# Optimization experiments

Measured on AMD Instinct MI355X. Metric: run time of the kernel, lower is better.

Reference implementation:

```python
import jax, jax.numpy as jnp
import numpy as np

N_NODES = 100000
N_EDGES = 1600000
IN_FEATS = 128
OUT_FEATS = 64


def setup_inputs() -> dict:
    key = jax.random.key(0)
    k1, k2, k3, k4 = jax.random.split(key, 4)
    feat = jax.random.normal(k1, (N_NODES, IN_FEATS), dtype=jnp.float32)
    W = jax.random.normal(k2, (IN_FEATS, OUT_FEATS), dtype=jnp.float32) * (1.0 / np.sqrt(IN_FEATS))
    src = jax.random.randint(k3, (N_EDGES,), 0, N_NODES, dtype=jnp.int64)
    dst = jax.random.randint(k4, (N_EDGES,), 0, N_NODES, dtype=jnp.int64)
    return {"feat": feat, "W": W, "src": src, "dst": dst}


def reference(feat, W, src, dst):
    # Linear projection (bias=False): homogeneous graph -> shared fc
    ft = feat @ W  # [N, out]

    # per-edge dot-product score: e_ij = <ft[src], ft[dst]>
    a = jnp.sum(ft[src] * ft[dst], axis=-1)  # [E]

    # edge softmax segmented by destination node (numerically stable)
    neg_inf = jnp.finfo(a.dtype).min
    m = jax.ops.segment_max(a, dst, num_segments=N_NODES)  # [N]
    m = jnp.where(m == neg_inf, 0.0, m)  # guard zero-in-degree nodes
    e = jnp.exp(a - m[dst])  # [E]
    s = jax.ops.segment_sum(e, dst, num_segments=N_NODES)  # [N]
    s = jnp.where(s == 0.0, 1.0, s)
    sa = e / s[dst]  # [E]

    # weighted scatter-sum aggregation: out[i] = sum_{j in N(i)} sa_ij * ft[j]
    rst = jax.ops.segment_sum(ft[src] * sa[:, None], dst, num_segments=N_NODES)
    return rst
```

## Files before the change

kernel.cpp:

```cpp
#include <hip/hip_runtime.h>
#include <hip/hip_fp16.h>
#include <math.h>

#define N_NODES 100000
#define N_EDGES 1600000
#define IN_F    128
#define OUT_F   64
#define K_BKT     196
#define BKT_SHIFT 9
#define BKT_NODES 512
#define BKT_CAP   10240
#define CHUNK     4096
#define PBLKS     ((N_EDGES + CHUNK - 1) / CHUNK)
#define LTILES    (N_NODES / 16)
#define LBLKS     ((LTILES + 3) / 4)

typedef _Float16 half8 __attribute__((ext_vector_type(8)));
typedef _Float16 h2 __attribute__((ext_vector_type(2)));
typedef _Float16 h4 __attribute__((ext_vector_type(4)));
typedef __fp16   q2v __attribute__((ext_vector_type(2)));
typedef float    f32x4 __attribute__((ext_vector_type(4)));

__device__ __forceinline__ float fdot2f(h2 a, h2 b, float c) {
#if __has_builtin(__builtin_amdgcn_fdot2)
    return __builtin_amdgcn_fdot2(__builtin_bit_cast(q2v, a), __builtin_bit_cast(q2v, b), c, false);
#else
    return (float)a[0] * (float)b[0] + (float)a[1] * (float)b[1] + c;
#endif
}

#if __has_builtin(__builtin_amdgcn_update_dpp)
#define DPP_ADD(x, ctrl)                                                                  \
    (x) += __builtin_bit_cast(float, __builtin_amdgcn_update_dpp(                         \
               0, __builtin_bit_cast(int, (x)), (ctrl), 0xF, 0xF, true))
#define REDUCE16(x) do { DPP_ADD(x, 0xB1); DPP_ADD(x, 0x4E); \
                         DPP_ADD(x, 0x141); DPP_ADD(x, 0x140); } while (0)
#else
#define REDUCE16(x) do { x += __shfl_xor(x, 1); x += __shfl_xor(x, 2); \
                         x += __shfl_xor(x, 4); x += __shfl_xor(x, 8); } while (0)
#endif


__global__ __launch_bounds__(256) void partition_linear_kernel(const int* __restrict__ src,
                                                               const int* __restrict__ dst,
                                                               unsigned* __restrict__ staging,
                                                               int* __restrict__ pcnt,
                                                               int* __restrict__ pbase,
                                                               const float* __restrict__ feat,
                                                               const float* __restrict__ W,
                                                               __half* __restrict__ fth) {
    __shared__ int hist[256], lbase[256], sc[256];
    __shared__ unsigned sval[CHUNK];
    int t = threadIdx.x;
    if (blockIdx.x < PBLKS) {
        hist[t] = 0;
        __syncthreads();
        int beg = blockIdx.x * CHUNK;
        int end = min(beg + CHUNK, N_EDGES);
        for (int i = beg + t; i < end; i += 256)
            atomicAdd(&hist[dst[i] >> BKT_SHIFT], 1);
        __syncthreads();
        int v = hist[t];
        sc[t] = v;
        __syncthreads();
        for (int off = 1; off < 256; off <<= 1) {
            int add = (t >= off) ? sc[t - off] : 0;
            __syncthreads();
            sc[t] += add;
            __syncthreads();
        }
        int lb = sc[t] - v;
        lbase[t] = lb;
        pcnt[blockIdx.x * 256 + t]  = v;
        pbase[blockIdx.x * 256 + t] = lb;
        hist[t] = 0;
        __syncthreads();
        for (int i = beg + t; i < end; i += 256) {
            int s = src[i], d = dst[i];
            int b = d >> BKT_SHIFT;
            int r = atomicAdd(&hist[b], 1);
            sval[lbase[b] + r] = (unsigned)s | ((unsigned)(d & (BKT_NODES - 1)) << 17);
        }
        __syncthreads();
        int n = end - beg;
        for (int p = t; p < n; p += 256)
            staging[(size_t)blockIdx.x * CHUNK + p] = sval[p];
        return;
    }
    int gwave = (blockIdx.x - PBLKS) * 4 + (t >> 6);
    if (gwave >= LTILES) return;
    int lane = t & 63;
    int m = lane & 15, kg = lane >> 4;
    int r0 = gwave * 16;

    half8 fb[4][4];
#pragma unroll
    for (int kb = 0; kb < 4; ++kb)
#pragma unroll
        for (int nb = 0; nb < 4; ++nb) {
            const float* wp = W + (size_t)(kb * 32 + kg * 8) * OUT_F + nb * 16 + m;
#pragma unroll
            for (int j = 0; j < 8; ++j)
                fb[kb][nb][j] = (_Float16)wp[j * OUT_F];
        }

    f32x4 acc[4];
#pragma unroll
    for (int nb = 0; nb < 4; ++nb) acc[nb] = (f32x4){0.f, 0.f, 0.f, 0.f};

#pragma unroll
    for (int kb = 0; kb < 4; ++kb) {
        const float4* ap = (const float4*)(feat + (size_t)(r0 + m) * IN_F + kb * 32 + kg * 8);
        float4 a0 = ap[0], a1 = ap[1];
        half8 fa = {(_Float16)a0.x, (_Float16)a0.y, (_Float16)a0.z, (_Float16)a0.w,
                    (_Float16)a1.x, (_Float16)a1.y, (_Float16)a1.z, (_Float16)a1.w};
#pragma unroll
        for (int nb = 0; nb < 4; ++nb)
            acc[nb] = __builtin_amdgcn_mfma_f32_16x16x32_f16(fa, fb[kb][nb], acc[nb], 0, 0, 0);
    }
#pragma unroll
    for (int nb = 0; nb < 4; ++nb)
#pragma unroll
        for (int i = 0; i < 4; ++i)
            fth[(size_t)(r0 + kg * 4 + i) * OUT_F + nb * 16 + m] = __float2half_rn(acc[nb][i]);
}

__global__ __launch_bounds__(1024) void place_kernel(const unsigned* __restrict__ staging,
                                                     const int* __restrict__ pcnt,
                                                     const int* __restrict__ pbase,
                                                     int* __restrict__ row_beg,
                                                     int* __restrict__ row_end,
                                                     int* __restrict__ edge_src) {
    __shared__ unsigned sbuf[BKT_CAP];
    __shared__ int exo[PBLKS];
    __shared__ int pbs[PBLKS];
    __shared__ int scnt[PBLKS];
    __shared__ int s512[512];
    __shared__ int cnt[BKT_NODES], lcur[BKT_NODES];
    __shared__ int ntot;
    int t = threadIdx.x;
    int b = blockIdx.x;

    int d = 0;
    if (t < PBLKS) { d = pcnt[t * 256 + b]; pbs[t] = pbase[t * 256 + b]; scnt[t] = d; }
    if (t < 512) { s512[t] = (t < PBLKS) ? d : 0; cnt[t] = 0; }
    __syncthreads();
    for (int off = 1; off < 512; off <<= 1) {
        int add = (t >= off && t < 512) ? s512[t - off] : 0;
        __syncthreads();
        if (t < 512) s512[t] += add;
        __syncthreads();
    }
    if (t < PBLKS) exo[t] = s512[t] - d;
    if (t == PBLKS - 1) ntot = s512[t];
    __syncthreads();
    int n = ntot;

    {
        int wid = t >> 6, ln = t & 63;
        for (int s = wid; s < PBLKS; s += 16) {
            int c = scnt[s], eo = exo[s];
            size_t gb = (size_t)s * CHUNK + pbs[s];
            for (int j = ln; j < c; j += 64)
                sbuf[eo + j] = staging[gb + j];
        }
    }
    __syncthreads();
    for (int i = t; i < n; i += 1024)
        atomicAdd(&cnt[sbuf[i] >> 17], 1);
    __syncthreads();
    int v = (t < 512) ? cnt[t] : 0;
    if (t < 512) s512[t] = v;
    __syncthreads();
    for (int off = 1; off < 512; off <<= 1) {
        int add = (t >= off && t < 512) ? s512[t - off] : 0;
        __syncthreads();
        if (t < 512) s512[t] += add;
        __syncthreads();
    }
    if (t < 512) {
        int b0 = b * BKT_CAP + s512[t] - v;
        lcur[t] = b0;
        int node = b * BKT_NODES + t;
        if (node < N_NODES) { row_beg[node] = b0; row_end[node] = b0 + v; }
    }
    __syncthreads();
    for (int i = t; i < n; i += 1024) {
        unsigned u = sbuf[i];
        int pos = atomicAdd(&lcur[u >> 17], 1);
        edge_src[pos] = (int)(u & 0x1FFFFu);
    }
}

__global__ __launch_bounds__(256) void fused_node_kernel(const __half* __restrict__ fth,
                                                         const int* __restrict__ row_beg,
                                                         const int* __restrict__ row_end,
                                                         const int* __restrict__ edge_src,
                                                         float* __restrict__ out) {
    const float LOG2E = 1.44269504088896340736f;
    int wave = (blockIdx.x * 256 + threadIdx.x) >> 6;
    int lane = threadIdx.x & 63;
    if (wave >= N_NODES) return;
    int q = lane >> 4, ql = lane & 15;

    int beg = row_beg[wave];
    int end = row_end[wave];

    const _Float16* fh = (const _Float16*)fth;
    h4 rdv = *(const h4*)(fh + (size_t)wave * OUT_F + 4 * ql);
    h2 dlo = __builtin_shufflevector(rdv, rdv, 0, 1);
    h2 dhi = __builtin_shufflevector(rdv, rdv, 2, 3);

    float m = -1e30f, l = 0.f;
    float a0 = 0.f, a1 = 0.f, a2 = 0.f, a3 = 0.f;

    for (int i = beg; i < end; i += 16) {
        int e0 = i + q, e1 = e0 + 4, e2 = e0 + 8, e3 = e0 + 12;
        bool u0 = e0 < end, u1 = e1 < end, u2 = e2 < end, u3 = e3 < end;
        int s0 = edge_src[u0 ? e0 : beg];
        int s1 = edge_src[u1 ? e1 : beg];
        int s2 = edge_src[u2 ? e2 : beg];
        int s3 = edge_src[u3 ? e3 : beg];
        h4 rA = *(const h4*)(fh + (size_t)s0 * OUT_F + 4 * ql);
        h4 rB = *(const h4*)(fh + (size_t)s1 * OUT_F + 4 * ql);
        h4 rC = *(const h4*)(fh + (size_t)s2 * OUT_F + 4 * ql);
        h4 rD = *(const h4*)(fh + (size_t)s3 * OUT_F + 4 * ql);

        float p0 = fdot2f(__builtin_shufflevector(rA, rA, 0, 1), dlo,
                   fdot2f(__builtin_shufflevector(rA, rA, 2, 3), dhi, 0.f));
        float p1 = fdot2f(__builtin_shufflevector(rB, rB, 0, 1), dlo,
                   fdot2f(__builtin_shufflevector(rB, rB, 2, 3), dhi, 0.f));
        float p2 = fdot2f(__builtin_shufflevector(rC, rC, 0, 1), dlo,
                   fdot2f(__builtin_shufflevector(rC, rC, 2, 3), dhi, 0.f));
        float p3 = fdot2f(__builtin_shufflevector(rD, rD, 0, 1), dlo,
                   fdot2f(__builtin_shufflevector(rD, rD, 2, 3), dhi, 0.f));
        REDUCE16(p0);
        REDUCE16(p1);
        REDUCE16(p2);
        REDUCE16(p3);
        p0 = u0 ? p0 * LOG2E : -1e30f;
        p1 = u1 ? p1 * LOG2E : -1e30f;
        p2 = u2 ? p2 * LOG2E : -1e30f;
        p3 = u3 ? p3 * LOG2E : -1e30f;

        float nm = fmaxf(fmaxf(fmaxf(p0, p1), fmaxf(p2, p3)), m);
        float alpha = exp2f(m - nm);
        float w0 = exp2f(p0 - nm), w1 = exp2f(p1 - nm);
        float w2 = exp2f(p2 - nm), w3 = exp2f(p3 - nm);
        l = l * alpha + ((w0 + w1) + (w2 + w3));
#if __has_builtin(__builtin_amdgcn_cvt_pkrtz)
        h2 wlo = __builtin_bit_cast(h2, __builtin_amdgcn_cvt_pkrtz(w0, w1));
        h2 whi = __builtin_bit_cast(h2, __builtin_amdgcn_cvt_pkrtz(w2, w3));
#else
        h2 wlo = {(_Float16)w0, (_Float16)w1};
        h2 whi = {(_Float16)w2, (_Float16)w3};
#endif
        h2 cab0 = {rA[0], rB[0]}, ccd0 = {rC[0], rD[0]};
        h2 cab1 = {rA[1], rB[1]}, ccd1 = {rC[1], rD[1]};
        h2 cab2 = {rA[2], rB[2]}, ccd2 = {rC[2], rD[2]};
        h2 cab3 = {rA[3], rB[3]}, ccd3 = {rC[3], rD[3]};
        a0 = fdot2f(wlo, cab0, fdot2f(whi, ccd0, a0 * alpha));
        a1 = fdot2f(wlo, cab1, fdot2f(whi, ccd1, a1 * alpha));
        a2 = fdot2f(wlo, cab2, fdot2f(whi, ccd2, a2 * alpha));
        a3 = fdot2f(wlo, cab3, fdot2f(whi, ccd3, a3 * alpha));
        m = nm;
    }

#pragma unroll
    for (int dd = 16; dd <= 32; dd <<= 1) {
        float m2 = __shfl_xor(m, dd), l2 = __shfl_xor(l, dd);
        float b0 = __shfl_xor(a0, dd), b1 = __shfl_xor(a1, dd);
        float b2 = __shfl_xor(a2, dd), b3 = __shfl_xor(a3, dd);
        float M = fmaxf(m, m2);
        float e1 = exp2f(m - M), e2 = exp2f(m2 - M);
        l = l * e1 + l2 * e2;
        a0 = a0 * e1 + b0 * e2;
        a1 = a1 * e1 + b1 * e2;
        a2 = a2 * e1 + b2 * e2;
        a3 = a3 * e1 + b3 * e2;
        m = M;
    }
    if (q == 0) {
        float inv = (l > 0.f) ? 1.f / l : 0.f;
        *(float4*)(out + (size_t)wave * OUT_F + 4 * ql) =
            make_float4(a0 * inv, a1 * inv, a2 * inv, a3 * inv);
    }
}

extern "C" void kernel_launch(void* const* d_in, const int* in_sizes, int n_in,
                              void* d_out, int out_size, void* d_ws, size_t ws_size,
                              hipStream_t stream) {
    const float* feat = (const float*)d_in[0];
    const float* W    = (const float*)d_in[1];
    const int*   src  = (const int*)d_in[2];
    const int*   dst  = (const int*)d_in[3];
    float* out = (float*)d_out;

    __half*   fth      = (__half*)d_ws;
    unsigned* staging  = (unsigned*)((int*)d_ws + (size_t)N_NODES * OUT_F / 2);
    int*      edge_src = (int*)(staging + (size_t)PBLKS * CHUNK);
    int*      pcnt     = edge_src + (size_t)K_BKT * BKT_CAP;
    int*      pbase    = pcnt + PBLKS * 256;
    int*      row_beg  = pbase + PBLKS * 256;
    int*      row_end  = row_beg + N_NODES;

    partition_linear_kernel<<<PBLKS + LBLKS, 256, 0, stream>>>(src, dst, staging, pcnt, pbase,
                                                               feat, W, fth);
    place_kernel<<<K_BKT, 1024, 0, stream>>>(staging, pcnt, pbase, row_beg, row_end, edge_src);
    fused_node_kernel<<<(N_NODES * 64) / 256, 256, 0, stream>>>(fth, row_beg, row_end, edge_src, out);
}
```

Measured before the change: 188.8 us.

## Fuse CSR placement with per-node attention aggregation using shared-memory CSR

Merges the bucket placement kernel and the per-node softmax-aggregation kernel into one. Each bucket is split into four quarter-blocks of 128 nodes. Every quarter-block reloads the full bucket staging into LDS, builds a local CSR in shared memory, and then has its 16 waves process 8 nodes each. This drops a kernel launch and the global edge_src/row_beg/row_end round trip. In exchange, each bucket's staging is read four times, occupancy drops to 784 large blocks with heavy LDS use, and a quarter's edges could overflow QCAP.

```diff
diff --git a/kernel.cpp b/kernel.cpp
--- a/kernel.cpp
+++ b/kernel.cpp
@@ -10,6 +10,7 @@
 #define BKT_SHIFT 9
 #define BKT_NODES 512
 #define BKT_CAP   10240
+#define QCAP      3072
 #define CHUNK     4096
 #define PBLKS     ((N_EDGES + CHUNK - 1) / CHUNK)
 #define LTILES    (N_NODES / 16)
@@ -125,25 +126,25 @@
             fth[(size_t)(r0 + kg * 4 + i) * OUT_F + nb * 16 + m] = __float2half_rn(acc[nb][i]);
 }
 
-__global__ __launch_bounds__(1024) void place_kernel(const unsigned* __restrict__ staging,
-                                                     const int* __restrict__ pcnt,
-                                                     const int* __restrict__ pbase,
-                                                     int* __restrict__ row_beg,
-                                                     int* __restrict__ row_end,
-                                                     int* __restrict__ edge_src) {
+__global__ __launch_bounds__(1024) void place_fused_kernel(const unsigned* __restrict__ staging,
+                                                           const int* __restrict__ pcnt,
+                                                           const int* __restrict__ pbase,
+                                                           const __half* __restrict__ fth,
+                                                           float* __restrict__ out) {
+    const float LOG2E = 1.44269504088896340736f;
     __shared__ unsigned sbuf[BKT_CAP];
-    __shared__ int exo[PBLKS];
-    __shared__ int pbs[PBLKS];
-    __shared__ int scnt[PBLKS];
+    __shared__ int exo[PBLKS], pbs[PBLKS], scnt[PBLKS];
     __shared__ int s512[512];
-    __shared__ int cnt[BKT_NODES], lcur[BKT_NODES];
+    __shared__ int cnt[128], rbeg[128], lcur[128];
+    __shared__ int csr[QCAP];
     __shared__ int ntot;
     int t = threadIdx.x;
-    int b = blockIdx.x;
+    int b = blockIdx.x >> 2, qb = blockIdx.x & 3;
 
     int d = 0;
     if (t < PBLKS) { d = pcnt[t * 256 + b]; pbs[t] = pbase[t * 256 + b]; scnt[t] = d; }
-    if (t < 512) { s512[t] = (t < PBLKS) ? d : 0; cnt[t] = 0; }
+    if (t < 512) s512[t] = (t < PBLKS) ? d : 0;
+    if (t < 128) cnt[t] = 0;
     __syncthreads();
     for (int off = 1; off < 512; off <<= 1) {
         int add = (t >= off && t < 512) ? s512[t - off] : 0;
@@ -166,124 +167,121 @@
         }
     }
     __syncthreads();
-    for (int i = t; i < n; i += 1024)
-        atomicAdd(&cnt[sbuf[i] >> 17], 1);
-    __syncthreads();
-    int v = (t < 512) ? cnt[t] : 0;
-    if (t < 512) s512[t] = v;
-    __syncthreads();
-    for (int off = 1; off < 512; off <<= 1) {
-        int add = (t >= off && t < 512) ? s512[t - off] : 0;
-        __syncthreads();
-        if (t < 512) s512[t] += add;
-        __syncthreads();
-    }
-    if (t < 512) {
-        int b0 = b * BKT_CAP + s512[t] - v;
-        lcur[t] = b0;
-        int node = b * BKT_NODES + t;
-        if (node < N_NODES) { row_beg[node] = b0; row_end[node] = b0 + v; }
-    }
+
+    for (int i = t; i < n; i += 1024) {
+        int nl = sbuf[i] >> 17;
+        if ((nl >> 7) == qb) atomicAdd(&cnt[nl & 127], 1);
+    }
+    __syncthreads();
+    if (t < 128) s512[t] = cnt[t];
+    __syncthreads();
+    for (int off = 1; off < 128; off <<= 1) {
+        int add = (t >= off && t < 128) ? s512[t - off] : 0;
+        __syncthreads();
+        if (t < 128) s512[t] += add;
+        __syncthreads();
+    }
+    if (t < 128) { int v = cnt[t]; int b0 = s512[t] - v; rbeg[t] = b0; lcur[t] = b0; }
     __syncthreads();
     for (int i = t; i < n; i += 1024) {
         unsigned u = sbuf[i];
-        int pos = atomicAdd(&lcur[u >> 17], 1);
-        edge_src[pos] = (int)(u & 0x1FFFFu);
-    }
-}
-
-__global__ __launch_bounds__(256) void fused_node_kernel(const __half* __restrict__ fth,
-                                                         const int* __restrict__ row_beg,
-                                                         const int* __restrict__ row_end,
-                                                         const int* __restrict__ edge_src,
-                                                         float* __restrict__ out) {
-    const float LOG2E = 1.44269504088896340736f;
-    int wave = (blockIdx.x * 256 + threadIdx.x) >> 6;
-    int lane = threadIdx.x & 63;
-    if (wave >= N_NODES) return;
+        int nl = u >> 17;
+        if ((nl >> 7) == qb) {
+            int pos = atomicAdd(&lcur[nl & 127], 1);
+            csr[pos] = (int)(u & 0x1FFFFu);
+        }
+    }
+    __syncthreads();
+
+    int wid = t >> 6, lane = t & 63;
     int q = lane >> 4, ql = lane & 15;
-
-    int beg = row_beg[wave];
-    int end = row_end[wave];
-
     const _Float16* fh = (const _Float16*)fth;
-    h4 rdv = *(const h4*)(fh + (size_t)wave * OUT_F + 4 * ql);
-    h2 dlo = __builtin_shufflevector(rdv, rdv, 0, 1);
-    h2 dhi = __builtin_shufflevector(rdv, rdv, 2, 3);
-
-    float m = -1e30f, l = 0.f;
-    float a0 = 0.f, a1 = 0.f, a2 = 0.f, a3 = 0.f;
-
-    for (int i = beg; i < end; i += 16) {
-        int e0 = i + q, e1 = e0 + 4, e2 = e0 + 8, e3 = e0 + 12;
-        bool u0 = e0 < end, u1 = e1 < end, u2 = e2 < end, u3 = e3 < end;
-        int s0 = edge_src[u0 ? e0 : beg];
-        int s1 = edge_src[u1 ? e1 : beg];
-        int s2 = edge_src[u2 ? e2 : beg];
-        int s3 = edge_src[u3 ? e3 : beg];
-        h4 rA = *(const h4*)(fh + (size_t)s0 * OUT_F + 4 * ql);
-        h4 rB = *(const h4*)(fh + (size_t)s1 * OUT_F + 4 * ql);
-        h4 rC = *(const h4*)(fh + (size_t)s2 * OUT_F + 4 * ql);
-        h4 rD = *(const h4*)(fh + (size_t)s3 * OUT_F + 4 * ql);
-
-        float p0 = fdot2f(__builtin_shufflevector(rA, rA, 0, 1), dlo,
-                   fdot2f(__builtin_shufflevector(rA, rA, 2, 3), dhi, 0.f));
-        float p1 = fdot2f(__builtin_shufflevector(rB, rB, 0, 1), dlo,
-                   fdot2f(__builtin_shufflevector(rB, rB, 2, 3), dhi, 0.f));
-        float p2 = fdot2f(__builtin_shufflevector(rC, rC, 0, 1), dlo,
-                   fdot2f(__builtin_shufflevector(rC, rC, 2, 3), dhi, 0.f));
-        float p3 = fdot2f(__builtin_shufflevector(rD, rD, 0, 1), dlo,
-                   fdot2f(__builtin_shufflevector(rD, rD, 2, 3), dhi, 0.f));
-        REDUCE16(p0);
-        REDUCE16(p1);
-        REDUCE16(p2);
-        REDUCE16(p3);
-        p0 = u0 ? p0 * LOG2E : -1e30f;
-        p1 = u1 ? p1 * LOG2E : -1e30f;
-        p2 = u2 ? p2 * LOG2E : -1e30f;
-        p3 = u3 ? p3 * LOG2E : -1e30f;
-
-        float nm = fmaxf(fmaxf(fmaxf(p0, p1), fmaxf(p2, p3)), m);
-        float alpha = exp2f(m - nm);
-        float w0 = exp2f(p0 - nm), w1 = exp2f(p1 - nm);
-        float w2 = exp2f(p2 - nm), w3 = exp2f(p3 - nm);
-        l = l * alpha + ((w0 + w1) + (w2 + w3));
+#pragma unroll
+    for (int k = 0; k < 8; ++k) {
+        int ln = wid + 16 * k;
+        int node = b * BKT_NODES + qb * 128 + ln;
+        int beg = rbeg[ln];
+        int end = beg + cnt[ln];
+
+        h4 rdv = (node < N_NODES)
+                   ? *(const h4*)(fh + (size_t)node * OUT_F + 4 * ql) : (h4){0, 0, 0, 0};
+        h2 dlo = __builtin_shufflevector(rdv, rdv, 0, 1);
+        h2 dhi = __builtin_shufflevector(rdv, rdv, 2, 3);
+
+        float m = -1e30f, l = 0.f;
+        float a0 = 0.f, a1 = 0.f, a2 = 0.f, a3 = 0.f;
+
+        for (int i = beg; i < end; i += 16) {
+            int e0 = i + q, e1 = e0 + 4, e2 = e0 + 8, e3 = e0 + 12;
+            bool u0 = e0 < end, u1 = e1 < end, u2 = e2 < end, u3 = e3 < end;
+            int s0 = csr[u0 ? e0 : beg];
+            int s1 = csr[u1 ? e1 : beg];
+            int s2 = csr[u2 ? e2 : beg];
+            int s3 = csr[u3 ? e3 : beg];
+            h4 rA = *(const h4*)(fh + (size_t)s0 * OUT_F + 4 * ql);
+            h4 rB = *(const h4*)(fh + (size_t)s1 * OUT_F + 4 * ql);
+            h4 rC = *(const h4*)(fh + (size_t)s2 * OUT_F + 4 * ql);
+            h4 rD = *(const h4*)(fh + (size_t)s3 * OUT_F + 4 * ql);
+
+            float p0 = fdot2f(__builtin_shufflevector(rA, rA, 0, 1), dlo,
+                       fdot2f(__builtin_shufflevector(rA, rA, 2, 3), dhi, 0.f));
+            float p1 = fdot2f(__builtin_shufflevector(rB, rB, 0, 1), dlo,
+                       fdot2f(__builtin_shufflevector(rB, rB, 2, 3), dhi, 0.f));
+            float p2 = fdot2f(__builtin_shufflevector(rC, rC, 0, 1), dlo,
+                       fdot2f(__builtin_shufflevector(rC, rC, 2, 3), dhi, 0.f));
+            float p3 = fdot2f(__builtin_shufflevector(rD, rD, 0, 1), dlo,
+                       fdot2f(__builtin_shufflevector(rD, rD, 2, 3), dhi, 0.f));
+            REDUCE16(p0);
+            REDUCE16(p1);
+            REDUCE16(p2);
+            REDUCE16(p3);
+            p0 = u0 ? p0 * LOG2E : -1e30f;
+            p1 = u1 ? p1 * LOG2E : -1e30f;
+            p2 = u2 ? p2 * LOG2E : -1e30f;
+            p3 = u3 ? p3 * LOG2E : -1e30f;
+
+            float nm = fmaxf(fmaxf(fmaxf(p0, p1), fmaxf(p2, p3)), m);
+            float alpha = exp2f(m - nm);
+            float w0 = exp2f(p0 - nm), w1 = exp2f(p1 - nm);
+            float w2 = exp2f(p2 - nm), w3 = exp2f(p3 - nm);
+            l = l * alpha + ((w0 + w1) + (w2 + w3));
 #if __has_builtin(__builtin_amdgcn_cvt_pkrtz)
-        h2 wlo = __builtin_bit_cast(h2, __builtin_amdgcn_cvt_pkrtz(w0, w1));
-        h2 whi = __builtin_bit_cast(h2, __builtin_amdgcn_cvt_pkrtz(w2, w3));
+            h2 wlo = __builtin_bit_cast(h2, __builtin_amdgcn_cvt_pkrtz(w0, w1));
+            h2 whi = __builtin_bit_cast(h2, __builtin_amdgcn_cvt_pkrtz(w2, w3));
 #else
-        h2 wlo = {(_Float16)w0, (_Float16)w1};
-        h2 whi = {(_Float16)w2, (_Float16)w3};
+            h2 wlo = {(_Float16)w0, (_Float16)w1};
+            h2 whi = {(_Float16)w2, (_Float16)w3};
 #endif
-        h2 cab0 = {rA[0], rB[0]}, ccd0 = {rC[0], rD[0]};
-        h2 cab1 = {rA[1], rB[1]}, ccd1 = {rC[1], rD[1]};
-        h2 cab2 = {rA[2], rB[2]}, ccd2 = {rC[2], rD[2]};
-        h2 cab3 = {rA[3], rB[3]}, ccd3 = {rC[3], rD[3]};
-        a0 = fdot2f(wlo, cab0, fdot2f(whi, ccd0, a0 * alpha));
-        a1 = fdot2f(wlo, cab1, fdot2f(whi, ccd1, a1 * alpha));
-        a2 = fdot2f(wlo, cab2, fdot2f(whi, ccd2, a2 * alpha));
-        a3 = fdot2f(wlo, cab3, fdot2f(whi, ccd3, a3 * alpha));
-        m = nm;
-    }
-
-#pragma unroll
-    for (int dd = 16; dd <= 32; dd <<= 1) {
-        float m2 = __shfl_xor(m, dd), l2 = __shfl_xor(l, dd);
-        float b0 = __shfl_xor(a0, dd), b1 = __shfl_xor(a1, dd);
-        float b2 = __shfl_xor(a2, dd), b3 = __shfl_xor(a3, dd);
-        float M = fmaxf(m, m2);
-        float e1 = exp2f(m - M), e2 = exp2f(m2 - M);
-        l = l * e1 + l2 * e2;
-        a0 = a0 * e1 + b0 * e2;
-        a1 = a1 * e1 + b1 * e2;
-        a2 = a2 * e1 + b2 * e2;
-        a3 = a3 * e1 + b3 * e2;
-        m = M;
-    }
-    if (q == 0) {
-        float inv = (l > 0.f) ? 1.f / l : 0.f;
-        *(float4*)(out + (size_t)wave * OUT_F + 4 * ql) =
-            make_float4(a0 * inv, a1 * inv, a2 * inv, a3 * inv);
+            h2 cab0 = {rA[0], rB[0]}, ccd0 = {rC[0], rD[0]};
+            h2 cab1 = {rA[1], rB[1]}, ccd1 = {rC[1], rD[1]};
+            h2 cab2 = {rA[2], rB[2]}, ccd2 = {rC[2], rD[2]};
+            h2 cab3 = {rA[3], rB[3]}, ccd3 = {rC[3], rD[3]};
+            a0 = fdot2f(wlo, cab0, fdot2f(whi, ccd0, a0 * alpha));
+            a1 = fdot2f(wlo, cab1, fdot2f(whi, ccd1, a1 * alpha));
+            a2 = fdot2f(wlo, cab2, fdot2f(whi, ccd2, a2 * alpha));
+            a3 = fdot2f(wlo, cab3, fdot2f(whi, ccd3, a3 * alpha));
+            m = nm;
+        }
+
+#pragma unroll
+        for (int dd = 16; dd <= 32; dd <<= 1) {
+            float m2 = __shfl_xor(m, dd), l2 = __shfl_xor(l, dd);
+            float b0 = __shfl_xor(a0, dd), b1 = __shfl_xor(a1, dd);
+            float b2 = __shfl_xor(a2, dd), b3 = __shfl_xor(a3, dd);
+            float M = fmaxf(m, m2);
+            float e1 = exp2f(m - M), e2 = exp2f(m2 - M);
+            l = l * e1 + l2 * e2;
+            a0 = a0 * e1 + b0 * e2;
+            a1 = a1 * e1 + b1 * e2;
+            a2 = a2 * e1 + b2 * e2;
+            a3 = a3 * e1 + b3 * e2;
+            m = M;
+        }
+        if (q == 0 && node < N_NODES) {
+            float inv = (l > 0.f) ? 1.f / l : 0.f;
+            *(float4*)(out + (size_t)node * OUT_F + 4 * ql) =
+                make_float4(a0 * inv, a1 * inv, a2 * inv, a3 * inv);
+        }
     }
 }
 
@@ -298,14 +296,10 @@
 
     __half*   fth      = (__half*)d_ws;
     unsigned* staging  = (unsigned*)((int*)d_ws + (size_t)N_NODES * OUT_F / 2);
-    int*      edge_src = (int*)(staging + (size_t)PBLKS * CHUNK);
-    int*      pcnt     = edge_src + (size_t)K_BKT * BKT_CAP;
+    int*      pcnt     = (int*)(staging + (size_t)PBLKS * CHUNK);
     int*      pbase    = pcnt + PBLKS * 256;
-    int*      row_beg  = pbase + PBLKS * 256;
-    int*      row_end  = row_beg + N_NODES;
 
     partition_linear_kernel<<<PBLKS + LBLKS, 256, 0, stream>>>(src, dst, staging, pcnt, pbase,
                                                                feat, W, fth);
-    place_kernel<<<K_BKT, 1024, 0, stream>>>(staging, pcnt, pbase, row_beg, row_end, edge_src);
-    fused_node_kernel<<<(N_NODES * 64) / 256, 256, 0, stream>>>(fth, row_beg, row_end, edge_src, out);
+    place_fused_kernel<<<K_BKT * 4, 1024, 0, stream>>>(staging, pcnt, pbase, fth, out);
 }
```

New measurement: 208.0 us. 10.2% more time.
